# Optimization experiments

Hardware: AMD Instinct MI355X
Metric: run time of the kernel (lower is better)

The kernel has to match this reference:

```python
import jax, jax.numpy as jnp
import numpy as np

B, S = 4, 4096          # batch, tokens (64x64 SAM ViT-H grid)
DIN, DOUT = 1280, 3840  # qkv linear dims
RANK = 16
NUM_SHARED = 1
NUM_ROUTED = 6
TOP_K = 3


def setup_inputs() -> dict:
    key = jax.random.key(0)
    ks = jax.random.split(key, 9)
    s = 0.02
    return {
        "x": jax.random.normal(ks[0], (B, S, DIN), dtype=jnp.float32),
        "base_w": jax.random.normal(ks[1], (DIN, DOUT), dtype=jnp.float32) * s,
        "base_b": jax.random.normal(ks[2], (DOUT,), dtype=jnp.float32) * s,
        "shared_w1": jax.random.normal(ks[3], (NUM_SHARED, DIN, RANK), dtype=jnp.float32) * s,
        "shared_w2": jax.random.normal(ks[4], (NUM_SHARED, RANK, DOUT), dtype=jnp.float32) * s,
        "routed_w1": jax.random.normal(ks[5], (NUM_ROUTED, DIN, RANK), dtype=jnp.float32) * s,
        "routed_w2": jax.random.normal(ks[6], (NUM_ROUTED, RANK, DOUT), dtype=jnp.float32) * s,
        "router_w": jax.random.normal(ks[7], (DIN, NUM_ROUTED), dtype=jnp.float32) * s,
        "router_b": jax.random.normal(ks[8], (NUM_ROUTED,), dtype=jnp.float32) * s,
    }


def reference(x, base_w, base_b, shared_w1, shared_w2, routed_w1, routed_w2, router_w, router_b):
    b, s, din = x.shape
    # base linear runs under torch.no_grad() -> stop_gradient
    base = jax.lax.stop_gradient(jnp.einsum('bsi,io->bso', x, base_w) + base_b)
    # shared low-rank experts, summed over the shared set
    shared = jnp.einsum('bsi,eir,ero->bso', x, shared_w1, shared_w2)
    # router: softmax gates, top-k selection
    gates = jax.nn.softmax(x @ router_w + router_b, axis=-1)      # [B,S,E]
    topk_w, topk_idx = jax.lax.top_k(gates, TOP_K)                # [B,S,K]
    T = b * s
    xf = x.reshape(T, din)
    # combine weights: per-token weight for each expert (top-k indices are
    # distinct, so scatter-add reproduces the per-slot assignment exactly)
    cw = jnp.zeros((T, NUM_ROUTED), dtype=x.dtype).at[
        jnp.arange(T)[:, None], topk_idx.reshape(T, TOP_K)
    ].add(topk_w.reshape(T, TOP_K))                               # [T,E]
    # routed experts: contract rank and expert dims without materializing [T,E,DOUT]
    h = jnp.einsum('ti,eir->ter', xf, routed_w1)                  # [T,E,RANK]
    routed = jnp.einsum('ter,ero,te->to', h, routed_w2, cw).reshape(b, s, DOUT)
    return base + shared + routed
```

## Files before the change

### kernel.cpp

```cpp
#include <hip/hip_runtime.h>
#include <cstdint>
#include <cstddef>

#define DIN 1280
#define DOUT 3840
#define NEXP 6
#define RANK 16
#define TOKENS 16384
#define KPAD 1408
#define NLOW 128

typedef __bf16 bf16x8 __attribute__((ext_vector_type(8)));
typedef float f32x4 __attribute__((ext_vector_type(4)));
typedef unsigned short u16x8 __attribute__((ext_vector_type(8)));

#define SB() __builtin_amdgcn_sched_barrier(0)
#define BAR() __builtin_amdgcn_s_barrier()

__device__ __forceinline__ unsigned short f2bf(float f) {
    unsigned u = __builtin_bit_cast(unsigned, f);
    u += 0x7fff + ((u >> 16) & 1);
    return (unsigned short)(u >> 16);
}

__device__ __forceinline__ void async_load16(void* lds, const void* g) {
    __builtin_amdgcn_global_load_lds(
        (const __attribute__((address_space(1))) unsigned int*)g,
        (__attribute__((address_space(3))) unsigned int*)lds, 16, 0, 0);
}

__global__ void prep_w2t(const float* __restrict__ base_w,
                         const float* __restrict__ shared_w2,
                         const float* __restrict__ routed_w2,
                         unsigned short* __restrict__ WT) {
    __shared__ unsigned short tile[32][33];
    int k0 = blockIdx.x * 32, n0 = blockIdx.y * 32;
    int tx = threadIdx.x, ty = threadIdx.y;
#pragma unroll
    for (int j = 0; j < 4; j++) {
        int k = k0 + ty + j * 8;
        int n = n0 + tx;
        float v;
        if (k < DIN)            v = base_w[(size_t)k * DOUT + n];
        else if (k < DIN + 16)  v = shared_w2[(size_t)(k - DIN) * DOUT + n];
        else if (k < DIN + 112) v = routed_w2[(size_t)(k - DIN - 16) * DOUT + n];
        else                    v = 0.f;
        tile[ty + j * 8][tx] = f2bf(v);
    }
    __syncthreads();
#pragma unroll
    for (int j = 0; j < 4; j++) {
        int n = n0 + ty + j * 8;
        int k = k0 + tx;
        WT[(size_t)n * KPAD + k] = tile[tx][ty + j * 8];
    }
}

__global__ void prep_w1t(const float* __restrict__ shared_w1,
                         const float* __restrict__ routed_w1,
                         unsigned short* __restrict__ W1T) {
    __shared__ unsigned short tile[32][33];
    int k0 = blockIdx.x * 32, n0 = blockIdx.y * 32;
    int tx = threadIdx.x, ty = threadIdx.y;
#pragma unroll
    for (int j = 0; j < 4; j++) {
        int k = k0 + ty + j * 8;
        int n = n0 + tx;
        float v = 0.f;
        if (n < 16) v = shared_w1[k * RANK + n];
        else if (n < 112) {
            int jj = n - 16, e = jj >> 4, r = jj & 15;
            v = routed_w1[(size_t)e * DIN * RANK + k * RANK + r];
        }
        tile[ty + j * 8][tx] = f2bf(v);
    }
    __syncthreads();
#pragma unroll
    for (int j = 0; j < 4; j++) {
        int n = n0 + ty + j * 8;
        int k = k0 + tx;
        W1T[(size_t)n * DIN + k] = tile[tx][ty + j * 8];
    }
}

__global__ __launch_bounds__(256) void router_kernel(
    const float* __restrict__ x,
    const float* __restrict__ router_w,
    const float* __restrict__ router_b,
    unsigned short* __restrict__ A,
    float* __restrict__ cw) {
    int tid = threadIdx.x;
    size_t t0 = (size_t)blockIdx.x * 8;
    const float* xblk = x + t0 * DIN;
    unsigned short* Ablk = A + t0 * KPAD;

    for (int i = tid; i < 8 * (DIN / 8); i += 256) {
        int t = i / (DIN / 8), c = (i - t * (DIN / 8)) * 8;
        const float* xs = xblk + (size_t)t * DIN + c;
        f32x4 v0 = *(const f32x4*)xs;
        f32x4 v1 = *(const f32x4*)(xs + 4);
        u16x8 o;
#pragma unroll
        for (int j = 0; j < 4; j++) { o[j] = f2bf(v0[j]); o[4 + j] = f2bf(v1[j]); }
        *(u16x8*)&Ablk[(size_t)t * KPAD + c] = o;
    }
    if (tid < 128) {
        int t = tid >> 4, c = tid & 15;
        Ablk[t * KPAD + DIN + 112 + c] = 0;
    }

    int tg = tid >> 5, lj = tid & 31;
    const float* xt = xblk + (size_t)tg * DIN;
    float acc[6] = {0.f, 0.f, 0.f, 0.f, 0.f, 0.f};
    for (int k = lj; k < DIN; k += 32) {
        float xv = xt[k];
        const float* wr = router_w + k * NEXP;
#pragma unroll
        for (int e = 0; e < NEXP; e++) acc[e] = fmaf(xv, wr[e], acc[e]);
    }
#pragma unroll
    for (int off = 16; off > 0; off >>= 1)
#pragma unroll
        for (int e = 0; e < NEXP; e++) acc[e] += __shfl_xor(acc[e], off);

    float mx = -1e30f;
#pragma unroll
    for (int e = 0; e < NEXP; e++) { acc[e] += router_b[e]; mx = fmaxf(mx, acc[e]); }
    float g[6]; float s = 0.f;
#pragma unroll
    for (int e = 0; e < NEXP; e++) { g[e] = __expf(acc[e] - mx); s += g[e]; }
    float inv = 1.f / s;
    if (lj < NEXP) {
        float ge = g[lj];
        int cnt = 0;
#pragma unroll
        for (int e = 0; e < NEXP; e++) {
            if (e == lj) continue;
            if (g[e] > ge || (g[e] == ge && e < lj)) cnt++;
        }
        cw[(t0 + tg) * NEXP + lj] = (cnt < 3) ? ge * inv : 0.f;
    }
}

__global__ __launch_bounds__(256) void combine_kernel(
    const float* __restrict__ H, const float* __restrict__ cw,
    unsigned short* __restrict__ A) {
    int i = blockIdx.x * 256 + threadIdx.x;
    int t = i / 112, j = i - t * 112;
    float h = H[(size_t)t * NLOW + j] + H[(size_t)TOKENS * NLOW + (size_t)t * NLOW + j];
    float f = (j < 16) ? 1.0f : cw[t * NEXP + ((j - 16) >> 4)];
    A[(size_t)t * KPAD + DIN + j] = f2bf(f * h);
}

__global__ __launch_bounds__(256, 2) void gemm_small(
    const unsigned short* __restrict__ A,
    const unsigned short* __restrict__ BT,
    float* __restrict__ H) {
    __shared__ unsigned short ldsA[128 * 32];
    __shared__ unsigned short ldsB[128 * 32];
    const int KS = DIN / 2;
    int tid = threadIdx.x;
    int lane = tid & 63, wave = tid >> 6;
    int m0 = blockIdx.y * 128;
    int z = blockIdx.z;
    int wm = (wave >> 1) * 64, wn = (wave & 1) * 64;
    int lr = lane & 15, quad = lane >> 4;

    f32x4 acc[4][4] = {};
    const unsigned short* Abase = A + (size_t)m0 * KPAD + z * KS;
    const unsigned short* Bbase = BT + z * KS;
    float* Cbase = H + (size_t)z * TOKENS * NLOW;

    for (int k0 = 0; k0 < KS; k0 += 32) {
#pragma unroll
        for (int i = 0; i < 2; i++) {
            int c = i * 256 + tid;
            int row = c >> 2;
            int col = (c & 3) << 3;
            async_load16(&ldsA[(i * 256 + wave * 64) * 8],
                         Abase + (size_t)row * KPAD + k0 + col);
            async_load16(&ldsB[(i * 256 + wave * 64) * 8],
                         Bbase + (size_t)row * DIN + k0 + col);
        }
        __syncthreads();
        bf16x8 af[4], bf[4];
#pragma unroll
        for (int mi = 0; mi < 4; mi++)
            af[mi] = *(const bf16x8*)&ldsA[(wm + mi * 16 + lr) * 32 + quad * 8];
#pragma unroll
        for (int ni = 0; ni < 4; ni++)
            bf[ni] = *(const bf16x8*)&ldsB[(wn + ni * 16 + lr) * 32 + quad * 8];
#pragma unroll
        for (int mi = 0; mi < 4; mi++)
#pragma unroll
            for (int ni = 0; ni < 4; ni++)
                acc[mi][ni] = __builtin_amdgcn_mfma_f32_16x16x32_bf16(
                    af[mi], bf[ni], acc[mi][ni], 0, 0, 0);
        __syncthreads();
    }
#pragma unroll
    for (int ni = 0; ni < 4; ni++) {
        int gn = wn + ni * 16 + lr;
#pragma unroll
        for (int mi = 0; mi < 4; mi++) {
            int gm = m0 + wm + mi * 16 + quad * 4;
            f32x4 v = acc[mi][ni];
#pragma unroll
            for (int r = 0; r < 4; r++)
                Cbase[(size_t)(gm + r) * NLOW + gn] = v[r];
        }
    }
}


#define READ_AQ(AQ, MB) do { \
    AQ[0][0] = rdA(a_cur, (MB) + 0, 0); AQ[0][1] = rdA(a_cur, (MB) + 0, 1); \
    AQ[1][0] = rdA(a_cur, (MB) + 1, 0); AQ[1][1] = rdA(a_cur, (MB) + 1, 1); \
} while (0)

#define MFMA_QUAD(AQ, MB) do { \
    _Pragma("unroll") for (int ks_ = 0; ks_ < 2; ks_++) \
    _Pragma("unroll") for (int mq_ = 0; mq_ < 2; mq_++) \
    _Pragma("unroll") for (int ni_ = 0; ni_ < 4; ni_++) \
        acc[(MB) + mq_][ni_] = __builtin_amdgcn_mfma_f32_16x16x32_bf16( \
            AQ[mq_][ks_], bfr[ni_][ks_], acc[(MB) + mq_][ni_], 0, 0, 0); \
} while (0)

__global__ __launch_bounds__(512, 2) void gemm256(
    const unsigned short* __restrict__ A,
    const unsigned short* __restrict__ BT,
    const float* __restrict__ bias,
    float* __restrict__ C) {
    __shared__ unsigned short lA[2][256 * 64];
    __shared__ unsigned short lB[2][256 * 64];

    int tid = threadIdx.x;
    int lane = tid & 63, wave = tid >> 6;
    int bid = blockIdx.x;
    int xcd = bid & 7, lid = bid >> 3;
    int mt = xcd * 8 + (lid & 7);
    int nt = lid >> 3;
    int m0 = mt * 256, n0 = nt * 256;

    int wm = (wave >> 2) * 128, wn = (wave & 3) * 64;
    int lr = lane & 15, quad = lane >> 4;
    int swz = (lr & 7) << 4;

    int sr = lane >> 3;
    int sc = (lane & 7) ^ sr;
    const unsigned short* aSrc = A + (size_t)(m0 + wave * 32 + sr) * KPAD + sc * 8;
    const unsigned short* bSrc = BT + (size_t)(n0 + wave * 32 + sr) * KPAD + sc * 8;

    auto stA4 = [&](unsigned short* dst, int k0) {
#pragma unroll
        for (int i = 0; i < 4; i++)
            async_load16(dst + (size_t)(wave * 32 + i * 8) * 64,
                         aSrc + (size_t)(i * 8) * KPAD + k0);
    };
    auto stB1 = [&](unsigned short* dst, int k0, int i) {
        async_load16(dst + (size_t)(wave * 32 + i * 8) * 64,
                     bSrc + (size_t)(i * 8) * KPAD + k0);
    };
    auto rdA = [&](const unsigned short* base, int mi, int ks) -> bf16x8 {
        int row = wm + mi * 16 + lr;
        int off = row * 128 + (((ks << 6) | (quad << 4)) ^ swz);
        return *(const bf16x8*)((const char*)base + off);
    };
    auto rdB = [&](const unsigned short* base, int ni, int ks) -> bf16x8 {
        int row = wn + ni * 16 + lr;
        int off = row * 128 + (((ks << 6) | (quad << 4)) ^ swz);
        return *(const bf16x8*)((const char*)base + off);
    };

    f32x4 acc[8][4] = {};

    stA4(&lA[0][0], 0);
#pragma unroll
    for (int i = 0; i < 4; i++) stB1(&lB[0][0], 0, i);
#pragma unroll
    for (int i = 0; i < 4; i++) stB1(&lB[1][0], 64, i);
    asm volatile("s_waitcnt vmcnt(4)" ::: "memory");
    SB(); BAR(); SB();

    const int nkt = KPAD / 64;
#pragma unroll 2
    for (int t = 0; t < nkt; ++t) {
        const int ct = t & 1;
        unsigned short* a_cur = &lA[ct][0];
        unsigned short* b_cur = &lB[ct][0];
        unsigned short* a_nxt = &lA[ct ^ 1][0];
        int k0 = t * 64;

        bf16x8 bfr[4][2];
#pragma unroll
        for (int ni = 0; ni < 4; ni++) {
            bfr[ni][0] = rdB(b_cur, ni, 0);
            bfr[ni][1] = rdB(b_cur, ni, 1);
        }
        SB();
        bf16x8 aq0[2][2], aq1[2][2], aq2[2][2], aq3[2][2];
        READ_AQ(aq0, 0);
        READ_AQ(aq1, 2);
        if (t + 1 < nkt) stA4(a_nxt, k0 + 64);

        READ_AQ(aq2, 4);
        __builtin_amdgcn_s_setprio(1); MFMA_QUAD(aq0, 0); __builtin_amdgcn_s_setprio(0);
        asm volatile("s_waitcnt lgkmcnt(8)" ::: "memory");
        SB(); BAR(); SB();

        READ_AQ(aq3, 6);
        if (t + 2 < nkt) { stB1(b_cur, k0 + 128, 0); stB1(b_cur, k0 + 128, 1); }
        __builtin_amdgcn_s_setprio(1); MFMA_QUAD(aq1, 2); __builtin_amdgcn_s_setprio(0);

        if (t + 2 < nkt) { stB1(b_cur, k0 + 128, 2); stB1(b_cur, k0 + 128, 3); }
        __builtin_amdgcn_s_setprio(1); MFMA_QUAD(aq2, 4); __builtin_amdgcn_s_setprio(0);

        __builtin_amdgcn_s_setprio(1); MFMA_QUAD(aq3, 6); __builtin_amdgcn_s_setprio(0);

        if (t + 2 < nkt) asm volatile("s_waitcnt vmcnt(4) lgkmcnt(0)" ::: "memory");
        else             asm volatile("s_waitcnt vmcnt(0) lgkmcnt(0)" ::: "memory");
        SB(); BAR(); SB();
    }

#pragma unroll
    for (int mi = 0; mi < 8; mi++) {
        int gm = m0 + wm + mi * 16 + quad * 4;
#pragma unroll
        for (int ni = 0; ni < 4; ni++) {
            int gn = n0 + wn + ni * 16 + lr;
            float bv = bias[gn];
            f32x4 v = acc[mi][ni];
#pragma unroll
            for (int r = 0; r < 4; r++)
                C[(size_t)(gm + r) * DOUT + gn] = v[r] + bv;
        }
    }
}

extern "C" void kernel_launch(void* const* d_in, const int* in_sizes, int n_in,
                              void* d_out, int out_size, void* d_ws, size_t ws_size,
                              hipStream_t stream) {
    const float* x         = (const float*)d_in[0];
    const float* base_w    = (const float*)d_in[1];
    const float* base_b    = (const float*)d_in[2];
    const float* shared_w1 = (const float*)d_in[3];
    const float* shared_w2 = (const float*)d_in[4];
    const float* routed_w1 = (const float*)d_in[5];
    const float* routed_w2 = (const float*)d_in[6];
    const float* router_w  = (const float*)d_in[7];
    const float* router_b  = (const float*)d_in[8];
    float* out = (float*)d_out;

    char* ws = (char*)d_ws;
    size_t off = 0;
    unsigned short* A     = (unsigned short*)(ws + off); off += (size_t)TOKENS * KPAD * 2;
    unsigned short* WcatT = (unsigned short*)(ws + off); off += (size_t)DOUT * KPAD * 2;
    unsigned short* W1T   = (unsigned short*)(ws + off); off += (size_t)NLOW * DIN * 2;
    float* H              = (float*)(ws + off);          off += (size_t)2 * TOKENS * NLOW * 4;
    float* cw             = (float*)(ws + off);          off += (size_t)TOKENS * NEXP * 4;

    prep_w2t<<<dim3(KPAD / 32, DOUT / 32), dim3(32, 8), 0, stream>>>(
        base_w, shared_w2, routed_w2, WcatT);
    prep_w1t<<<dim3(DIN / 32, NLOW / 32), dim3(32, 8), 0, stream>>>(
        shared_w1, routed_w1, W1T);
    router_kernel<<<TOKENS / 8, 256, 0, stream>>>(x, router_w, router_b, A, cw);
    gemm_small<<<dim3(1, TOKENS / 128, 2), 256, 0, stream>>>(A, W1T, H);
    combine_kernel<<<(TOKENS * 112) / 256, 256, 0, stream>>>(H, cw, A);
    gemm256<<<(TOKENS / 256) * (DOUT / 256), 512, 0, stream>>>(A, WcatT, base_b, out);
}
```

Measured before the change: 284.9 us.

## Restructure GEMM main loop into 4-phase ping-pong schedule with split A/B prefetch

Reworks the gemm256 K-loop into four phases. Each phase reads one A quad from LDS, issues half of a next-tile A or B async load, hits a barrier, waits lgkmcnt(0), runs the MFMA quad, and barriers again. The prologue now also prefetches A for the second stage, so A gets a two-stage prefetch just as B already had. The aim is to spread global loads evenly and interleave wave groups in a ping-pong style so MFMA issue overlaps memory traffic. The cost is many more barriers per K step and smaller register buffering, since only one A quad is live at a time.

```diff
diff --git a/kernel.cpp b/kernel.cpp
--- a/kernel.cpp
+++ b/kernel.cpp
@@ -226,6 +226,8 @@
             AQ[mq_][ks_], bfr[ni_][ks_], acc[(MB) + mq_][ni_], 0, 0, 0); \
 } while (0)
 
+#define LGKM0() do { asm volatile("s_waitcnt lgkmcnt(0)" ::: "memory"); SB(); } while (0)
+
 __global__ __launch_bounds__(512, 2) void gemm256(
     const unsigned short* __restrict__ A,
     const unsigned short* __restrict__ BT,
@@ -251,15 +253,17 @@
     const unsigned short* aSrc = A + (size_t)(m0 + wave * 32 + sr) * KPAD + sc * 8;
     const unsigned short* bSrc = BT + (size_t)(n0 + wave * 32 + sr) * KPAD + sc * 8;
 
-    auto stA4 = [&](unsigned short* dst, int k0) {
-#pragma unroll
-        for (int i = 0; i < 4; i++)
+    auto stA2 = [&](unsigned short* dst, int k0, int pr) {
+#pragma unroll
+        for (int i = pr * 2; i < pr * 2 + 2; i++)
             async_load16(dst + (size_t)(wave * 32 + i * 8) * 64,
                          aSrc + (size_t)(i * 8) * KPAD + k0);
     };
-    auto stB1 = [&](unsigned short* dst, int k0, int i) {
-        async_load16(dst + (size_t)(wave * 32 + i * 8) * 64,
-                     bSrc + (size_t)(i * 8) * KPAD + k0);
+    auto stB2 = [&](unsigned short* dst, int k0, int pr) {
+#pragma unroll
+        for (int i = pr * 2; i < pr * 2 + 2; i++)
+            async_load16(dst + (size_t)(wave * 32 + i * 8) * 64,
+                         bSrc + (size_t)(i * 8) * KPAD + k0);
     };
     auto rdA = [&](const unsigned short* base, int mi, int ks) -> bf16x8 {
         int row = wm + mi * 16 + lr;
@@ -274,51 +278,56 @@
 
     f32x4 acc[8][4] = {};
 
-    stA4(&lA[0][0], 0);
-#pragma unroll
-    for (int i = 0; i < 4; i++) stB1(&lB[0][0], 0, i);
-#pragma unroll
-    for (int i = 0; i < 4; i++) stB1(&lB[1][0], 64, i);
-    asm volatile("s_waitcnt vmcnt(4)" ::: "memory");
+    stA2(&lA[0][0], 0, 0);  stA2(&lA[0][0], 0, 1);
+    stB2(&lB[0][0], 0, 0);  stB2(&lB[0][0], 0, 1);
+    stA2(&lA[1][0], 64, 0); stA2(&lA[1][0], 64, 1);
+    stB2(&lB[1][0], 64, 0); stB2(&lB[1][0], 64, 1);
+    asm volatile("s_waitcnt vmcnt(8)" ::: "memory");
     SB(); BAR(); SB();
 
     const int nkt = KPAD / 64;
 #pragma unroll 2
     for (int t = 0; t < nkt; ++t) {
-        const int ct = t & 1;
-        unsigned short* a_cur = &lA[ct][0];
-        unsigned short* b_cur = &lB[ct][0];
-        unsigned short* a_nxt = &lA[ct ^ 1][0];
+        const int c = t & 1;
+        unsigned short* a_cur = &lA[c][0];
+        unsigned short* b_cur = &lB[c][0];
+        unsigned short* a_nxt = &lA[c ^ 1][0];
         int k0 = t * 64;
+        const bool stA_ok = (t >= 1) && (t + 1 < nkt);
+        const bool stB_ok = (t + 2 < nkt);
 
         bf16x8 bfr[4][2];
+        bf16x8 aq[2][2];
+
 #pragma unroll
         for (int ni = 0; ni < 4; ni++) {
             bfr[ni][0] = rdB(b_cur, ni, 0);
             bfr[ni][1] = rdB(b_cur, ni, 1);
         }
-        SB();
-        bf16x8 aq0[2][2], aq1[2][2], aq2[2][2], aq3[2][2];
-        READ_AQ(aq0, 0);
-        READ_AQ(aq1, 2);
-        if (t + 1 < nkt) stA4(a_nxt, k0 + 64);
-
-        READ_AQ(aq2, 4);
-        __builtin_amdgcn_s_setprio(1); MFMA_QUAD(aq0, 0); __builtin_amdgcn_s_setprio(0);
-        asm volatile("s_waitcnt lgkmcnt(8)" ::: "memory");
-        SB(); BAR(); SB();
-
-        READ_AQ(aq3, 6);
-        if (t + 2 < nkt) { stB1(b_cur, k0 + 128, 0); stB1(b_cur, k0 + 128, 1); }
-        __builtin_amdgcn_s_setprio(1); MFMA_QUAD(aq1, 2); __builtin_amdgcn_s_setprio(0);
-
-        if (t + 2 < nkt) { stB1(b_cur, k0 + 128, 2); stB1(b_cur, k0 + 128, 3); }
-        __builtin_amdgcn_s_setprio(1); MFMA_QUAD(aq2, 4); __builtin_amdgcn_s_setprio(0);
-
-        __builtin_amdgcn_s_setprio(1); MFMA_QUAD(aq3, 6); __builtin_amdgcn_s_setprio(0);
-
-        if (t + 2 < nkt) asm volatile("s_waitcnt vmcnt(4) lgkmcnt(0)" ::: "memory");
-        else             asm volatile("s_waitcnt vmcnt(0) lgkmcnt(0)" ::: "memory");
+        READ_AQ(aq, 0);
+        if (stA_ok) stA2(a_nxt, k0 + 64, 0);
+        SB(); BAR(); LGKM0();
+        __builtin_amdgcn_s_setprio(1); MFMA_QUAD(aq, 0); __builtin_amdgcn_s_setprio(0);
+        SB(); BAR();
+
+        READ_AQ(aq, 2);
+        if (stA_ok) stA2(a_nxt, k0 + 64, 1);
+        SB(); BAR(); LGKM0();
+        __builtin_amdgcn_s_setprio(1); MFMA_QUAD(aq, 2); __builtin_amdgcn_s_setprio(0);
+        SB(); BAR();
+
+        READ_AQ(aq, 4);
+        if (stB_ok) stB2(b_cur, k0 + 128, 0);
+        SB(); BAR(); LGKM0();
+        __builtin_amdgcn_s_setprio(1); MFMA_QUAD(aq, 4); __builtin_amdgcn_s_setprio(0);
+        SB(); BAR();
+
+        READ_AQ(aq, 6);
+        if (stB_ok) stB2(b_cur, k0 + 128, 1);
+        SB(); BAR(); LGKM0();
+        __builtin_amdgcn_s_setprio(1); MFMA_QUAD(aq, 6); __builtin_amdgcn_s_setprio(0);
+        if (stB_ok) asm volatile("s_waitcnt vmcnt(4)" ::: "memory");
+        else        asm volatile("s_waitcnt vmcnt(0)" ::: "memory");
         SB(); BAR(); SB();
     }
 
```

New measurement: 295.9 us. 1.04x slower.

## Prefetch A and B tiles two stages ahead with a reordered barrier schedule

Applied to the files above, without the earlier changes.

The GEMM main loop now prefetches both the A and B tiles two k-steps ahead into the double buffer, where before only A was loaded one step ahead. B loads are split into pairs interleaved with the MFMA quads. A loads for step t+2 are issued into the current buffer after an extra barrier that ensures all A reads have finished. This is meant to hide more global-load latency behind MFMA work, at the cost of an additional barrier per iteration and more in-flight loads (vmcnt 8).

```diff
diff --git a/kernel.cpp b/kernel.cpp
--- a/kernel.cpp
+++ b/kernel.cpp
@@ -251,15 +251,17 @@
     const unsigned short* aSrc = A + (size_t)(m0 + wave * 32 + sr) * KPAD + sc * 8;
     const unsigned short* bSrc = BT + (size_t)(n0 + wave * 32 + sr) * KPAD + sc * 8;
 
-    auto stA4 = [&](unsigned short* dst, int k0) {
-#pragma unroll
-        for (int i = 0; i < 4; i++)
+    auto stA2 = [&](unsigned short* dst, int k0, int pr) {
+#pragma unroll
+        for (int i = pr * 2; i < pr * 2 + 2; i++)
             async_load16(dst + (size_t)(wave * 32 + i * 8) * 64,
                          aSrc + (size_t)(i * 8) * KPAD + k0);
     };
-    auto stB1 = [&](unsigned short* dst, int k0, int i) {
-        async_load16(dst + (size_t)(wave * 32 + i * 8) * 64,
-                     bSrc + (size_t)(i * 8) * KPAD + k0);
+    auto stB2 = [&](unsigned short* dst, int k0, int pr) {
+#pragma unroll
+        for (int i = pr * 2; i < pr * 2 + 2; i++)
+            async_load16(dst + (size_t)(wave * 32 + i * 8) * 64,
+                         bSrc + (size_t)(i * 8) * KPAD + k0);
     };
     auto rdA = [&](const unsigned short* base, int mi, int ks) -> bf16x8 {
         int row = wm + mi * 16 + lr;
@@ -274,51 +276,60 @@
 
     f32x4 acc[8][4] = {};
 
-    stA4(&lA[0][0], 0);
-#pragma unroll
-    for (int i = 0; i < 4; i++) stB1(&lB[0][0], 0, i);
-#pragma unroll
-    for (int i = 0; i < 4; i++) stB1(&lB[1][0], 64, i);
-    asm volatile("s_waitcnt vmcnt(4)" ::: "memory");
+    stA2(&lA[0][0], 0, 0);  stA2(&lA[0][0], 0, 1);
+    stB2(&lB[0][0], 0, 0);  stB2(&lB[0][0], 0, 1);
+    stA2(&lA[1][0], 64, 0); stA2(&lA[1][0], 64, 1);
+    stB2(&lB[1][0], 64, 0); stB2(&lB[1][0], 64, 1);
+    asm volatile("s_waitcnt vmcnt(8)" ::: "memory");
     SB(); BAR(); SB();
 
     const int nkt = KPAD / 64;
 #pragma unroll 2
     for (int t = 0; t < nkt; ++t) {
-        const int ct = t & 1;
-        unsigned short* a_cur = &lA[ct][0];
-        unsigned short* b_cur = &lB[ct][0];
-        unsigned short* a_nxt = &lA[ct ^ 1][0];
+        const int c = t & 1;
+        unsigned short* a_cur = &lA[c][0];
+        unsigned short* b_cur = &lB[c][0];
         int k0 = t * 64;
+        const bool st_ok = (t + 2 < nkt);
 
         bf16x8 bfr[4][2];
+        bf16x8 aq0[2][2], aq1[2][2], aq2[2][2], aq3[2][2];
+
 #pragma unroll
         for (int ni = 0; ni < 4; ni++) {
             bfr[ni][0] = rdB(b_cur, ni, 0);
             bfr[ni][1] = rdB(b_cur, ni, 1);
         }
         SB();
-        bf16x8 aq0[2][2], aq1[2][2], aq2[2][2], aq3[2][2];
         READ_AQ(aq0, 0);
         READ_AQ(aq1, 2);
-        if (t + 1 < nkt) stA4(a_nxt, k0 + 64);
-
-        READ_AQ(aq2, 4);
-        __builtin_amdgcn_s_setprio(1); MFMA_QUAD(aq0, 0); __builtin_amdgcn_s_setprio(0);
+        SB();
         asm volatile("s_waitcnt lgkmcnt(8)" ::: "memory");
         SB(); BAR(); SB();
 
+        READ_AQ(aq2, 4);
+        if (st_ok) stB2(b_cur, k0 + 128, 0);
+        SB();
+        __builtin_amdgcn_s_setprio(1); MFMA_QUAD(aq0, 0); __builtin_amdgcn_s_setprio(0);
+        SB();
+
         READ_AQ(aq3, 6);
-        if (t + 2 < nkt) { stB1(b_cur, k0 + 128, 0); stB1(b_cur, k0 + 128, 1); }
+        if (st_ok) stB2(b_cur, k0 + 128, 1);
+        SB();
         __builtin_amdgcn_s_setprio(1); MFMA_QUAD(aq1, 2); __builtin_amdgcn_s_setprio(0);
-
-        if (t + 2 < nkt) { stB1(b_cur, k0 + 128, 2); stB1(b_cur, k0 + 128, 3); }
+        SB();
+
         __builtin_amdgcn_s_setprio(1); MFMA_QUAD(aq2, 4); __builtin_amdgcn_s_setprio(0);
-
+        SB();
+        asm volatile("s_waitcnt lgkmcnt(0)" ::: "memory");
+        SB(); BAR(); SB();
+
+        if (st_ok) { stA2(a_cur, k0 + 128, 0); stA2(a_cur, k0 + 128, 1); }
+        SB();
         __builtin_amdgcn_s_setprio(1); MFMA_QUAD(aq3, 6); __builtin_amdgcn_s_setprio(0);
-
-        if (t + 2 < nkt) asm volatile("s_waitcnt vmcnt(4) lgkmcnt(0)" ::: "memory");
-        else             asm volatile("s_waitcnt vmcnt(0) lgkmcnt(0)" ::: "memory");
+        SB();
+        if (st_ok) asm volatile("s_waitcnt vmcnt(8)" ::: "memory");
+        else       asm volatile("s_waitcnt vmcnt(0)" ::: "memory");
         SB(); BAR(); SB();
     }
 
```

Result: no change. 287.2 us (+0.8%).

## Rewrite main GEMM with 256x128 tiles, BK=32 and simple double buffering

Applied to the files above, without the earlier changes.

Replaces the hand-scheduled 256x256, BK=64 GEMM with a 256x128 tile, BK=32 kernel. It uses a plain one-barrier-per-step double buffer with an XOR swizzle and asks for four blocks per CU. The aim is more resident blocks and a simpler pipeline with less LDS per block. In exchange each block reuses the A tile across fewer output columns, so global traffic rises, and barriers happen twice as often. The interleaved MFMA/load scheduling and priority hints of the old kernel are lost.

```diff
diff --git a/kernel.cpp b/kernel.cpp
--- a/kernel.cpp
+++ b/kernel.cpp
@@ -13,9 +13,6 @@
 typedef __bf16 bf16x8 __attribute__((ext_vector_type(8)));
 typedef float f32x4 __attribute__((ext_vector_type(4)));
 typedef unsigned short u16x8 __attribute__((ext_vector_type(8)));
-
-#define SB() __builtin_amdgcn_sched_barrier(0)
-#define BAR() __builtin_amdgcn_s_barrier()
 
 __device__ __forceinline__ unsigned short f2bf(float f) {
     unsigned u = __builtin_bit_cast(unsigned, f);
@@ -213,26 +210,17 @@
 }
 
 
-#define READ_AQ(AQ, MB) do { \
-    AQ[0][0] = rdA(a_cur, (MB) + 0, 0); AQ[0][1] = rdA(a_cur, (MB) + 0, 1); \
-    AQ[1][0] = rdA(a_cur, (MB) + 1, 0); AQ[1][1] = rdA(a_cur, (MB) + 1, 1); \
-} while (0)
-
-#define MFMA_QUAD(AQ, MB) do { \
-    _Pragma("unroll") for (int ks_ = 0; ks_ < 2; ks_++) \
-    _Pragma("unroll") for (int mq_ = 0; mq_ < 2; mq_++) \
-    _Pragma("unroll") for (int ni_ = 0; ni_ < 4; ni_++) \
-        acc[(MB) + mq_][ni_] = __builtin_amdgcn_mfma_f32_16x16x32_bf16( \
-            AQ[mq_][ks_], bfr[ni_][ks_], acc[(MB) + mq_][ni_], 0, 0, 0); \
-} while (0)
-
-__global__ __launch_bounds__(512, 2) void gemm256(
+#define BM 256
+#define BN 128
+#define BKS 32
+
+__global__ __launch_bounds__(512, 4) void gemm256(
     const unsigned short* __restrict__ A,
     const unsigned short* __restrict__ BT,
     const float* __restrict__ bias,
     float* __restrict__ C) {
-    __shared__ unsigned short lA[2][256 * 64];
-    __shared__ unsigned short lB[2][256 * 64];
+    __shared__ unsigned short lA[2][BM * BKS];
+    __shared__ unsigned short lB[2][BN * BKS];
 
     int tid = threadIdx.x;
     int lane = tid & 63, wave = tid >> 6;
@@ -240,90 +228,61 @@
     int xcd = bid & 7, lid = bid >> 3;
     int mt = xcd * 8 + (lid & 7);
     int nt = lid >> 3;
-    int m0 = mt * 256, n0 = nt * 256;
-
-    int wm = (wave >> 2) * 128, wn = (wave & 3) * 64;
+    int m0 = mt * BM, n0 = nt * BN;
+
+    int wm = (wave >> 1) * 64, wn = (wave & 1) * 64;
     int lr = lane & 15, quad = lane >> 4;
-    int swz = (lr & 7) << 4;
-
-    int sr = lane >> 3;
-    int sc = (lane & 7) ^ sr;
-    const unsigned short* aSrc = A + (size_t)(m0 + wave * 32 + sr) * KPAD + sc * 8;
-    const unsigned short* bSrc = BT + (size_t)(n0 + wave * 32 + sr) * KPAD + sc * 8;
-
-    auto stA4 = [&](unsigned short* dst, int k0) {
-#pragma unroll
-        for (int i = 0; i < 4; i++)
-            async_load16(dst + (size_t)(wave * 32 + i * 8) * 64,
-                         aSrc + (size_t)(i * 8) * KPAD + k0);
-    };
-    auto stB1 = [&](unsigned short* dst, int k0, int i) {
-        async_load16(dst + (size_t)(wave * 32 + i * 8) * 64,
-                     bSrc + (size_t)(i * 8) * KPAD + k0);
-    };
-    auto rdA = [&](const unsigned short* base, int mi, int ks) -> bf16x8 {
-        int row = wm + mi * 16 + lr;
-        int off = row * 128 + (((ks << 6) | (quad << 4)) ^ swz);
-        return *(const bf16x8*)((const char*)base + off);
-    };
-    auto rdB = [&](const unsigned short* base, int ni, int ks) -> bf16x8 {
-        int row = wn + ni * 16 + lr;
-        int off = row * 128 + (((ks << 6) | (quad << 4)) ^ swz);
-        return *(const bf16x8*)((const char*)base + off);
-    };
-
-    f32x4 acc[8][4] = {};
-
-    stA4(&lA[0][0], 0);
-#pragma unroll
-    for (int i = 0; i < 4; i++) stB1(&lB[0][0], 0, i);
-#pragma unroll
-    for (int i = 0; i < 4; i++) stB1(&lB[1][0], 64, i);
-    asm volatile("s_waitcnt vmcnt(4)" ::: "memory");
-    SB(); BAR(); SB();
-
-    const int nkt = KPAD / 64;
+
+    int srow = tid >> 2;
+    int scg = (tid & 3) ^ ((tid >> 3) & 3);
+    const unsigned short* aSrc = A + (size_t)(m0 + srow) * KPAD + scg * 8;
+    const unsigned short* bSrc = BT + (size_t)(n0 + srow) * KPAD + scg * 8;
+
+    f32x4 acc[4][4] = {};
+
+    const int nkt = KPAD / BKS;
+    {
+        async_load16(&lA[0][0] + (size_t)tid * 8, aSrc);
+        async_load16(&lA[0][0] + 128 * BKS + (size_t)tid * 8, aSrc + (size_t)128 * KPAD);
+        async_load16(&lB[0][0] + (size_t)tid * 8, bSrc);
+    }
+
 #pragma unroll 2
     for (int t = 0; t < nkt; ++t) {
-        const int ct = t & 1;
-        unsigned short* a_cur = &lA[ct][0];
-        unsigned short* b_cur = &lB[ct][0];
-        unsigned short* a_nxt = &lA[ct ^ 1][0];
-        int k0 = t * 64;
-
-        bf16x8 bfr[4][2];
+        __syncthreads();
+        if (t + 1 < nkt) {
+            int k1 = (t + 1) * BKS;
+            unsigned short* dA = &lA[(t + 1) & 1][0];
+            unsigned short* dB = &lB[(t + 1) & 1][0];
+            async_load16(dA + (size_t)tid * 8, aSrc + k1);
+            async_load16(dA + 128 * BKS + (size_t)tid * 8, aSrc + (size_t)128 * KPAD + k1);
+            async_load16(dB + (size_t)tid * 8, bSrc + k1);
+        }
+        const unsigned short* a_cur = &lA[t & 1][0];
+        const unsigned short* b_cur = &lB[t & 1][0];
+        bf16x8 af[4], bf[4];
+#pragma unroll
+        for (int mi = 0; mi < 4; mi++) {
+            int row = wm + mi * 16 + lr;
+            int off = row * 64 + (((quad ^ ((row >> 1) & 3))) << 4);
+            af[mi] = *(const bf16x8*)((const char*)a_cur + off);
+        }
 #pragma unroll
         for (int ni = 0; ni < 4; ni++) {
-            bfr[ni][0] = rdB(b_cur, ni, 0);
-            bfr[ni][1] = rdB(b_cur, ni, 1);
-        }
-        SB();
-        bf16x8 aq0[2][2], aq1[2][2], aq2[2][2], aq3[2][2];
-        READ_AQ(aq0, 0);
-        READ_AQ(aq1, 2);
-        if (t + 1 < nkt) stA4(a_nxt, k0 + 64);
-
-        READ_AQ(aq2, 4);
-        __builtin_amdgcn_s_setprio(1); MFMA_QUAD(aq0, 0); __builtin_amdgcn_s_setprio(0);
-        asm volatile("s_waitcnt lgkmcnt(8)" ::: "memory");
-        SB(); BAR(); SB();
-
-        READ_AQ(aq3, 6);
-        if (t + 2 < nkt) { stB1(b_cur, k0 + 128, 0); stB1(b_cur, k0 + 128, 1); }
-        __builtin_amdgcn_s_setprio(1); MFMA_QUAD(aq1, 2); __builtin_amdgcn_s_setprio(0);
-
-        if (t + 2 < nkt) { stB1(b_cur, k0 + 128, 2); stB1(b_cur, k0 + 128, 3); }
-        __builtin_amdgcn_s_setprio(1); MFMA_QUAD(aq2, 4); __builtin_amdgcn_s_setprio(0);
-
-        __builtin_amdgcn_s_setprio(1); MFMA_QUAD(aq3, 6); __builtin_amdgcn_s_setprio(0);
-
-        if (t + 2 < nkt) asm volatile("s_waitcnt vmcnt(4) lgkmcnt(0)" ::: "memory");
-        else             asm volatile("s_waitcnt vmcnt(0) lgkmcnt(0)" ::: "memory");
-        SB(); BAR(); SB();
-    }
-
-#pragma unroll
-    for (int mi = 0; mi < 8; mi++) {
+            int row = wn + ni * 16 + lr;
+            int off = row * 64 + (((quad ^ ((row >> 1) & 3))) << 4);
+            bf[ni] = *(const bf16x8*)((const char*)b_cur + off);
+        }
+#pragma unroll
+        for (int mi = 0; mi < 4; mi++)
+#pragma unroll
+            for (int ni = 0; ni < 4; ni++)
+                acc[mi][ni] = __builtin_amdgcn_mfma_f32_16x16x32_bf16(
+                    af[mi], bf[ni], acc[mi][ni], 0, 0, 0);
+    }
+
+#pragma unroll
+    for (int mi = 0; mi < 4; mi++) {
         int gm = m0 + wm + mi * 16 + quad * 4;
 #pragma unroll
         for (int ni = 0; ni < 4; ni++) {
@@ -366,5 +325,6 @@
     router_kernel<<<TOKENS / 8, 256, 0, stream>>>(x, router_w, router_b, A, cw);
     gemm_small<<<dim3(1, TOKENS / 128, 2), 256, 0, stream>>>(A, W1T, H);
     combine_kernel<<<(TOKENS * 112) / 256, 256, 0, stream>>>(H, cw, A);
-    gemm256<<<(TOKENS / 256) * (DOUT / 256), 512, 0, stream>>>(A, WcatT, base_b, out);
-}
+    gemm256<<<(DOUT / BN) * (TOKENS / BM), 512, 0, stream>>>(
+        A, WcatT, base_b, out);
+}
```

New measurement: 305.8 us. 1.07x slower.
